# Optimization experiments

Measured on AMD Instinct MI355X. Metric: run time of the kernel, lower is better.

The kernel has to match this reference:

```python
import jax, jax.numpy as jnp
import numpy as np

N_NODES = 16384


def gcn_conv(x, W, b, src, dst, n):
    # PyG GCNConv: h = D^{-1/2} (A + I) D^{-1/2} (x W) + b, edge weights = 1
    h = x @ W  # [N, C_out]
    ones = jnp.ones(src.shape[0], dtype=x.dtype)
    deg = jax.ops.segment_sum(ones, dst, num_segments=n) + 1.0  # +1 for self-loop
    inv_sqrt = jax.lax.rsqrt(deg)
    coef = inv_sqrt[src] * inv_sqrt[dst]  # [E]
    agg = jax.ops.segment_sum(h[src] * coef[:, None], dst, num_segments=n)
    agg = agg + h * (inv_sqrt * inv_sqrt)[:, None]  # self-loop term
    return agg + b


def setup_inputs() -> dict:
    key = jax.random.key(0)
    k_x, k_e, k_w1, k_w2 = jax.random.split(key, 4)
    n, e = N_NODES, 524288
    c_in, c_hid, c_out = 128, 64, 16
    x = jax.random.normal(k_x, (n, c_in), dtype=jnp.float32)
    edge_index = jax.random.randint(k_e, (2, e), 0, n, dtype=jnp.int64)
    adj = jnp.zeros((n, n), dtype=jnp.float32)  # unused in forward (only in loss())
    s1 = 1.0 / np.sqrt(c_in)
    s2 = 1.0 / np.sqrt(c_hid)
    W1 = jax.random.uniform(k_w1, (c_in, c_hid), minval=-s1, maxval=s1, dtype=jnp.float32)
    b1 = jnp.zeros((c_hid,), dtype=jnp.float32)
    W2 = jax.random.uniform(k_w2, (c_hid, c_out), minval=-s2, maxval=s2, dtype=jnp.float32)
    b2 = jnp.zeros((c_out,), dtype=jnp.float32)
    return {"x": x, "edge_index": edge_index, "adj": adj,
            "W1": W1, "b1": b1, "W2": W2, "b2": b2}


def reference(x, edge_index, adj, W1, b1, W2, b2):
    n = x.shape[0]
    src, dst = edge_index[0], edge_index[1]
    h = jax.nn.relu(gcn_conv(x, W1, b1, src, dst, n))
    logits = gcn_conv(h, W2, b2, src, dst, n)
    return jax.nn.softmax(logits, axis=1)
```

## Files before the change

### kernel.cpp

```cpp
#include <hip/hip_runtime.h>
#include <math.h>

#define N_NODES 16384
#define N_EDGES 524288
#define C_IN    128
#define C_HID   64
#define C_OUT   16
#define CAP     128

__global__ __launch_bounds__(256) void k_gemm1_bin(const float* __restrict__ x,
                                                   const float* __restrict__ W1,
                                                   float* __restrict__ h1,
                                                   const int* __restrict__ src,
                                                   const int* __restrict__ dst,
                                                   int* __restrict__ cnt,
                                                   int* __restrict__ csr) {
    __shared__ float sW[C_IN][C_HID];
    __shared__ float sx[16][C_IN];
    int tid = threadIdx.x;
    int e = (blockIdx.x * 256 + tid) * 2;

    int2 s2 = *(const int2*)&src[e];
    int2 d2 = *(const int2*)&dst[e];
    int slot0 = atomicAdd(&cnt[d2.x], 1);
    int slot1 = atomicAdd(&cnt[d2.y], 1);
    if (slot0 < CAP) csr[d2.x * CAP + slot0] = s2.x;
    if (slot1 < CAP) csr[d2.y * CAP + slot1] = s2.y;

    const float4* W4 = (const float4*)W1;
    float4* sW4 = (float4*)sW;
    for (int i = tid; i < C_IN * C_HID / 4; i += 256) sW4[i] = W4[i];
    const float4* x4 = (const float4*)(x + (size_t)blockIdx.x * 16 * C_IN);
    float4* sx4 = (float4*)sx;
    for (int i = tid; i < 16 * C_IN / 4; i += 256) sx4[i] = x4[i];
    __syncthreads();

    int w = tid >> 6, col = tid & 63;
    float a0 = 0.f, a1 = 0.f, a2 = 0.f, a3 = 0.f;
#pragma unroll 8
    for (int k = 0; k < C_IN; ++k) {
        float wv = sW[k][col];
        a0 = fmaf(sx[w][k],      wv, a0);
        a1 = fmaf(sx[w + 4][k],  wv, a1);
        a2 = fmaf(sx[w + 8][k],  wv, a2);
        a3 = fmaf(sx[w + 12][k], wv, a3);
    }
    int node0 = blockIdx.x * 16;
    h1[(node0 + w) * C_HID + col]      = a0;
    h1[(node0 + w + 4) * C_HID + col]  = a1;
    h1[(node0 + w + 8) * C_HID + col]  = a2;
    h1[(node0 + w + 12) * C_HID + col] = a3;
}

__global__ __launch_bounds__(256) void k_l1(const float* __restrict__ h1,
                                            const int* __restrict__ csr,
                                            const int* __restrict__ cnt,
                                            const float* __restrict__ b1,
                                            const float* __restrict__ W2,
                                            float* __restrict__ h2) {
    __shared__ float sW[C_OUT][C_HID + 1];
    __shared__ float sz[4][C_HID];
    int tid = threadIdx.x;
    for (int i = tid; i < C_HID * C_OUT; i += 256) {
        int k = i >> 4, c = i & 15;
        sW[c][k] = W2[i];
    }
    __syncthreads();

    int w = tid >> 6, lane = tid & 63;
    int node = blockIdx.x * 4 + w;
    int degf = cnt[node];
    int deg = degf < CAP ? degf : CAP;
    int sub = lane >> 4;
    int cq  = lane & 15;
    int cbase = node * CAP;

    float4 acc = make_float4(0.f, 0.f, 0.f, 0.f);
    for (int j = sub; j < deg; j += 4) {
        int s = csr[cbase + j];
        float iv = rsqrtf((float)cnt[s] + 1.0f);
        const float4 v = *(const float4*)&h1[s * C_HID + 4 * cq];
        acc.x = fmaf(v.x, iv, acc.x);
        acc.y = fmaf(v.y, iv, acc.y);
        acc.z = fmaf(v.z, iv, acc.z);
        acc.w = fmaf(v.w, iv, acc.w);
    }
    acc.x += __shfl_xor(acc.x, 16); acc.y += __shfl_xor(acc.y, 16);
    acc.z += __shfl_xor(acc.z, 16); acc.w += __shfl_xor(acc.w, 16);
    acc.x += __shfl_xor(acc.x, 32); acc.y += __shfl_xor(acc.y, 32);
    acc.z += __shfl_xor(acc.z, 32); acc.w += __shfl_xor(acc.w, 32);

    float ivd = rsqrtf((float)degf + 1.0f);
    float iv2 = ivd * ivd;
    const float4 self = *(const float4*)&h1[node * C_HID + 4 * cq];
    const float4 bb   = *(const float4*)&b1[4 * cq];
    if (lane < 16) {
        sz[w][4 * cq]     = fmaxf(fmaf(acc.x, ivd, fmaf(self.x, iv2, bb.x)), 0.f);
        sz[w][4 * cq + 1] = fmaxf(fmaf(acc.y, ivd, fmaf(self.y, iv2, bb.y)), 0.f);
        sz[w][4 * cq + 2] = fmaxf(fmaf(acc.z, ivd, fmaf(self.z, iv2, bb.z)), 0.f);
        sz[w][4 * cq + 3] = fmaxf(fmaf(acc.w, ivd, fmaf(self.w, iv2, bb.w)), 0.f);
    }
    int c = lane & 15, kg = lane >> 4;
    float p = 0.f;
#pragma unroll
    for (int i = 0; i < 16; ++i) {
        int k = kg * 16 + i;
        p += sz[w][k] * sW[c][k];
    }
    p += __shfl_xor(p, 16);
    p += __shfl_xor(p, 32);
    if (kg == 0) h2[node * C_OUT + c] = p;
}

__global__ __launch_bounds__(256) void k_l2(const float* __restrict__ h2,
                                            const int* __restrict__ csr,
                                            const int* __restrict__ cnt,
                                            const float* __restrict__ b2,
                                            float* __restrict__ out) {
    int tid = threadIdx.x;
    int w = tid >> 6, lane = tid & 63;
    int node = blockIdx.x * 4 + w;
    int degf = cnt[node];
    int deg = degf < CAP ? degf : CAP;
    int g  = lane >> 2;
    int cq = lane & 3;
    int cbase = node * CAP;

    float4 acc = make_float4(0.f, 0.f, 0.f, 0.f);
    for (int j = g; j < deg; j += 16) {
        int s = csr[cbase + j];
        float iv = rsqrtf((float)cnt[s] + 1.0f);
        const float4 v = *(const float4*)&h2[s * C_OUT + 4 * cq];
        acc.x = fmaf(v.x, iv, acc.x);
        acc.y = fmaf(v.y, iv, acc.y);
        acc.z = fmaf(v.z, iv, acc.z);
        acc.w = fmaf(v.w, iv, acc.w);
    }
#pragma unroll
    for (int d = 4; d < 64; d <<= 1) {
        acc.x += __shfl_xor(acc.x, d); acc.y += __shfl_xor(acc.y, d);
        acc.z += __shfl_xor(acc.z, d); acc.w += __shfl_xor(acc.w, d);
    }

    float ivd = rsqrtf((float)degf + 1.0f);
    float iv2 = ivd * ivd;
    const float4 self = *(const float4*)&h2[node * C_OUT + 4 * cq];
    const float4 bb   = *(const float4*)&b2[4 * cq];
    float l0  = fmaf(acc.x, ivd, fmaf(self.x, iv2, bb.x));
    float l1v = fmaf(acc.y, ivd, fmaf(self.y, iv2, bb.y));
    float l2v = fmaf(acc.z, ivd, fmaf(self.z, iv2, bb.z));
    float l3  = fmaf(acc.w, ivd, fmaf(self.w, iv2, bb.w));

    float mx = fmaxf(fmaxf(l0, l1v), fmaxf(l2v, l3));
    mx = fmaxf(mx, __shfl_xor(mx, 1));
    mx = fmaxf(mx, __shfl_xor(mx, 2));
    float e0 = expf(l0 - mx), e1 = expf(l1v - mx);
    float e2 = expf(l2v - mx), e3 = expf(l3 - mx);
    float sum = e0 + e1 + e2 + e3;
    sum += __shfl_xor(sum, 1);
    sum += __shfl_xor(sum, 2);
    float r = 1.0f / sum;
    if (lane < 4) {
        float4 o = make_float4(e0 * r, e1 * r, e2 * r, e3 * r);
        *(float4*)&out[node * C_OUT + 4 * cq] = o;
    }
}

extern "C" void kernel_launch(void* const* d_in, const int* in_sizes, int n_in,
                              void* d_out, int out_size, void* d_ws, size_t ws_size,
                              hipStream_t stream) {
    const float* x    = (const float*)d_in[0];
    const int*   eidx = (const int*)d_in[1];
    const float* W1   = (const float*)d_in[3];
    const float* b1   = (const float*)d_in[4];
    const float* W2   = (const float*)d_in[5];
    const float* b2   = (const float*)d_in[6];
    float* out = (float*)d_out;

    const int* src = eidx;
    const int* dst = eidx + N_EDGES;

    char* ws = (char*)d_ws;
    int*   cnt = (int*)  (ws);
    int*   csr = (int*)  (ws + (1 << 20));
    float* h1  = (float*)(ws + (16 << 20));
    float* h2  = (float*)(ws + (24 << 20));

    hipMemsetAsync(cnt, 0, (size_t)N_NODES * sizeof(int), stream);

    k_gemm1_bin<<<N_NODES / 16, 256, 0, stream>>>(x, W1, h1, src, dst, cnt, csr);
    k_l1<<<N_NODES / 4, 256, 0, stream>>>(h1, csr, cnt, b1, W2, h2);
    k_l2<<<N_NODES / 4, 256, 0, stream>>>(h2, csr, cnt, b2, out);
}
```

Baseline: 73.74 us.

## Coarsen GEMM/binning and aggregation kernels, replace memset with zero kernel

The fused GEMM+edge-binning kernel now handles 4 edges per thread and 32 nodes per block, reusing each W1 element across 8 rows. The two aggregation kernels loop over 4 groups of nodes per block, so there are fewer blocks and the W2 shared-memory staging is amortised. The memset is replaced by a small zeroing kernel. The aim is to cut per-block setup, W1 reloads and launch overhead, at the cost of fewer blocks, so less parallelism for hiding gather latency.

```diff
diff --git a/kernel.cpp b/kernel.cpp
--- a/kernel.cpp
+++ b/kernel.cpp
@@ -7,6 +7,10 @@
 #define C_HID   64
 #define C_OUT   16
 #define CAP     128
+
+__global__ __launch_bounds__(256) void k_zero(int4* __restrict__ cnt4) {
+    cnt4[blockIdx.x * 256 + threadIdx.x] = make_int4(0, 0, 0, 0);
+}
 
 __global__ __launch_bounds__(256) void k_gemm1_bin(const float* __restrict__ x,
                                                    const float* __restrict__ W1,
@@ -16,40 +20,42 @@
                                                    int* __restrict__ cnt,
                                                    int* __restrict__ csr) {
     __shared__ float sW[C_IN][C_HID];
-    __shared__ float sx[16][C_IN];
+    __shared__ float sx[32][C_IN];
     int tid = threadIdx.x;
-    int e = (blockIdx.x * 256 + tid) * 2;
-
-    int2 s2 = *(const int2*)&src[e];
-    int2 d2 = *(const int2*)&dst[e];
-    int slot0 = atomicAdd(&cnt[d2.x], 1);
-    int slot1 = atomicAdd(&cnt[d2.y], 1);
-    if (slot0 < CAP) csr[d2.x * CAP + slot0] = s2.x;
-    if (slot1 < CAP) csr[d2.y * CAP + slot1] = s2.y;
+    int e = (blockIdx.x * 256 + tid) * 4;
+
+    int4 s4 = *(const int4*)&src[e];
+    int4 d4 = *(const int4*)&dst[e];
+    int sl0 = atomicAdd(&cnt[d4.x], 1);
+    int sl1 = atomicAdd(&cnt[d4.y], 1);
+    int sl2 = atomicAdd(&cnt[d4.z], 1);
+    int sl3 = atomicAdd(&cnt[d4.w], 1);
+    if (sl0 < CAP) csr[d4.x * CAP + sl0] = s4.x;
+    if (sl1 < CAP) csr[d4.y * CAP + sl1] = s4.y;
+    if (sl2 < CAP) csr[d4.z * CAP + sl2] = s4.z;
+    if (sl3 < CAP) csr[d4.w * CAP + sl3] = s4.w;
 
     const float4* W4 = (const float4*)W1;
     float4* sW4 = (float4*)sW;
     for (int i = tid; i < C_IN * C_HID / 4; i += 256) sW4[i] = W4[i];
-    const float4* x4 = (const float4*)(x + (size_t)blockIdx.x * 16 * C_IN);
+    const float4* x4 = (const float4*)(x + (size_t)blockIdx.x * 32 * C_IN);
     float4* sx4 = (float4*)sx;
-    for (int i = tid; i < 16 * C_IN / 4; i += 256) sx4[i] = x4[i];
+    for (int i = tid; i < 32 * C_IN / 4; i += 256) sx4[i] = x4[i];
     __syncthreads();
 
     int w = tid >> 6, col = tid & 63;
-    float a0 = 0.f, a1 = 0.f, a2 = 0.f, a3 = 0.f;
-#pragma unroll 8
+    float a[8] = {0.f, 0.f, 0.f, 0.f, 0.f, 0.f, 0.f, 0.f};
+#pragma unroll 4
     for (int k = 0; k < C_IN; ++k) {
         float wv = sW[k][col];
-        a0 = fmaf(sx[w][k],      wv, a0);
-        a1 = fmaf(sx[w + 4][k],  wv, a1);
-        a2 = fmaf(sx[w + 8][k],  wv, a2);
-        a3 = fmaf(sx[w + 12][k], wv, a3);
-    }
-    int node0 = blockIdx.x * 16;
-    h1[(node0 + w) * C_HID + col]      = a0;
-    h1[(node0 + w + 4) * C_HID + col]  = a1;
-    h1[(node0 + w + 8) * C_HID + col]  = a2;
-    h1[(node0 + w + 12) * C_HID + col] = a3;
+#pragma unroll
+        for (int i = 0; i < 8; ++i)
+            a[i] = fmaf(sx[w + 4 * i][k], wv, a[i]);
+    }
+    int node0 = blockIdx.x * 32;
+#pragma unroll
+    for (int i = 0; i < 8; ++i)
+        h1[(node0 + w + 4 * i) * C_HID + col] = a[i];
 }
 
 __global__ __launch_bounds__(256) void k_l1(const float* __restrict__ h1,
@@ -68,48 +74,51 @@
     __syncthreads();
 
     int w = tid >> 6, lane = tid & 63;
-    int node = blockIdx.x * 4 + w;
-    int degf = cnt[node];
-    int deg = degf < CAP ? degf : CAP;
     int sub = lane >> 4;
     int cq  = lane & 15;
-    int cbase = node * CAP;
-
-    float4 acc = make_float4(0.f, 0.f, 0.f, 0.f);
-    for (int j = sub; j < deg; j += 4) {
-        int s = csr[cbase + j];
-        float iv = rsqrtf((float)cnt[s] + 1.0f);
-        const float4 v = *(const float4*)&h1[s * C_HID + 4 * cq];
-        acc.x = fmaf(v.x, iv, acc.x);
-        acc.y = fmaf(v.y, iv, acc.y);
-        acc.z = fmaf(v.z, iv, acc.z);
-        acc.w = fmaf(v.w, iv, acc.w);
-    }
-    acc.x += __shfl_xor(acc.x, 16); acc.y += __shfl_xor(acc.y, 16);
-    acc.z += __shfl_xor(acc.z, 16); acc.w += __shfl_xor(acc.w, 16);
-    acc.x += __shfl_xor(acc.x, 32); acc.y += __shfl_xor(acc.y, 32);
-    acc.z += __shfl_xor(acc.z, 32); acc.w += __shfl_xor(acc.w, 32);
-
-    float ivd = rsqrtf((float)degf + 1.0f);
-    float iv2 = ivd * ivd;
-    const float4 self = *(const float4*)&h1[node * C_HID + 4 * cq];
-    const float4 bb   = *(const float4*)&b1[4 * cq];
-    if (lane < 16) {
-        sz[w][4 * cq]     = fmaxf(fmaf(acc.x, ivd, fmaf(self.x, iv2, bb.x)), 0.f);
-        sz[w][4 * cq + 1] = fmaxf(fmaf(acc.y, ivd, fmaf(self.y, iv2, bb.y)), 0.f);
-        sz[w][4 * cq + 2] = fmaxf(fmaf(acc.z, ivd, fmaf(self.z, iv2, bb.z)), 0.f);
-        sz[w][4 * cq + 3] = fmaxf(fmaf(acc.w, ivd, fmaf(self.w, iv2, bb.w)), 0.f);
-    }
     int c = lane & 15, kg = lane >> 4;
-    float p = 0.f;
-#pragma unroll
-    for (int i = 0; i < 16; ++i) {
-        int k = kg * 16 + i;
-        p += sz[w][k] * sW[c][k];
-    }
-    p += __shfl_xor(p, 16);
-    p += __shfl_xor(p, 32);
-    if (kg == 0) h2[node * C_OUT + c] = p;
+
+    for (int it = 0; it < 4; ++it) {
+        int node = blockIdx.x * 16 + it * 4 + w;
+        int degf = cnt[node];
+        int deg = degf < CAP ? degf : CAP;
+        int cbase = node * CAP;
+
+        float4 acc = make_float4(0.f, 0.f, 0.f, 0.f);
+        for (int j = sub; j < deg; j += 4) {
+            int s = csr[cbase + j];
+            float iv = rsqrtf((float)cnt[s] + 1.0f);
+            const float4 v = *(const float4*)&h1[s * C_HID + 4 * cq];
+            acc.x = fmaf(v.x, iv, acc.x);
+            acc.y = fmaf(v.y, iv, acc.y);
+            acc.z = fmaf(v.z, iv, acc.z);
+            acc.w = fmaf(v.w, iv, acc.w);
+        }
+        acc.x += __shfl_xor(acc.x, 16); acc.y += __shfl_xor(acc.y, 16);
+        acc.z += __shfl_xor(acc.z, 16); acc.w += __shfl_xor(acc.w, 16);
+        acc.x += __shfl_xor(acc.x, 32); acc.y += __shfl_xor(acc.y, 32);
+        acc.z += __shfl_xor(acc.z, 32); acc.w += __shfl_xor(acc.w, 32);
+
+        float ivd = rsqrtf((float)degf + 1.0f);
+        float iv2 = ivd * ivd;
+        const float4 self = *(const float4*)&h1[node * C_HID + 4 * cq];
+        const float4 bb   = *(const float4*)&b1[4 * cq];
+        if (lane < 16) {
+            sz[w][4 * cq]     = fmaxf(fmaf(acc.x, ivd, fmaf(self.x, iv2, bb.x)), 0.f);
+            sz[w][4 * cq + 1] = fmaxf(fmaf(acc.y, ivd, fmaf(self.y, iv2, bb.y)), 0.f);
+            sz[w][4 * cq + 2] = fmaxf(fmaf(acc.z, ivd, fmaf(self.z, iv2, bb.z)), 0.f);
+            sz[w][4 * cq + 3] = fmaxf(fmaf(acc.w, ivd, fmaf(self.w, iv2, bb.w)), 0.f);
+        }
+        float p = 0.f;
+#pragma unroll
+        for (int i = 0; i < 16; ++i) {
+            int k = kg * 16 + i;
+            p += sz[w][k] * sW[c][k];
+        }
+        p += __shfl_xor(p, 16);
+        p += __shfl_xor(p, 32);
+        if (kg == 0) h2[node * C_OUT + c] = p;
+    }
 }
 
 __global__ __launch_bounds__(256) void k_l2(const float* __restrict__ h2,
@@ -119,50 +128,53 @@
                                             float* __restrict__ out) {
     int tid = threadIdx.x;
     int w = tid >> 6, lane = tid & 63;
-    int node = blockIdx.x * 4 + w;
-    int degf = cnt[node];
-    int deg = degf < CAP ? degf : CAP;
     int g  = lane >> 2;
     int cq = lane & 3;
-    int cbase = node * CAP;
-
-    float4 acc = make_float4(0.f, 0.f, 0.f, 0.f);
-    for (int j = g; j < deg; j += 16) {
-        int s = csr[cbase + j];
-        float iv = rsqrtf((float)cnt[s] + 1.0f);
-        const float4 v = *(const float4*)&h2[s * C_OUT + 4 * cq];
-        acc.x = fmaf(v.x, iv, acc.x);
-        acc.y = fmaf(v.y, iv, acc.y);
-        acc.z = fmaf(v.z, iv, acc.z);
-        acc.w = fmaf(v.w, iv, acc.w);
-    }
-#pragma unroll
-    for (int d = 4; d < 64; d <<= 1) {
-        acc.x += __shfl_xor(acc.x, d); acc.y += __shfl_xor(acc.y, d);
-        acc.z += __shfl_xor(acc.z, d); acc.w += __shfl_xor(acc.w, d);
-    }
-
-    float ivd = rsqrtf((float)degf + 1.0f);
-    float iv2 = ivd * ivd;
-    const float4 self = *(const float4*)&h2[node * C_OUT + 4 * cq];
-    const float4 bb   = *(const float4*)&b2[4 * cq];
-    float l0  = fmaf(acc.x, ivd, fmaf(self.x, iv2, bb.x));
-    float l1v = fmaf(acc.y, ivd, fmaf(self.y, iv2, bb.y));
-    float l2v = fmaf(acc.z, ivd, fmaf(self.z, iv2, bb.z));
-    float l3  = fmaf(acc.w, ivd, fmaf(self.w, iv2, bb.w));
-
-    float mx = fmaxf(fmaxf(l0, l1v), fmaxf(l2v, l3));
-    mx = fmaxf(mx, __shfl_xor(mx, 1));
-    mx = fmaxf(mx, __shfl_xor(mx, 2));
-    float e0 = expf(l0 - mx), e1 = expf(l1v - mx);
-    float e2 = expf(l2v - mx), e3 = expf(l3 - mx);
-    float sum = e0 + e1 + e2 + e3;
-    sum += __shfl_xor(sum, 1);
-    sum += __shfl_xor(sum, 2);
-    float r = 1.0f / sum;
-    if (lane < 4) {
-        float4 o = make_float4(e0 * r, e1 * r, e2 * r, e3 * r);
-        *(float4*)&out[node * C_OUT + 4 * cq] = o;
+
+    for (int it = 0; it < 4; ++it) {
+        int node = blockIdx.x * 16 + it * 4 + w;
+        int degf = cnt[node];
+        int deg = degf < CAP ? degf : CAP;
+        int cbase = node * CAP;
+
+        float4 acc = make_float4(0.f, 0.f, 0.f, 0.f);
+        for (int j = g; j < deg; j += 16) {
+            int s = csr[cbase + j];
+            float iv = rsqrtf((float)cnt[s] + 1.0f);
+            const float4 v = *(const float4*)&h2[s * C_OUT + 4 * cq];
+            acc.x = fmaf(v.x, iv, acc.x);
+            acc.y = fmaf(v.y, iv, acc.y);
+            acc.z = fmaf(v.z, iv, acc.z);
+            acc.w = fmaf(v.w, iv, acc.w);
+        }
+#pragma unroll
+        for (int d = 4; d < 64; d <<= 1) {
+            acc.x += __shfl_xor(acc.x, d); acc.y += __shfl_xor(acc.y, d);
+            acc.z += __shfl_xor(acc.z, d); acc.w += __shfl_xor(acc.w, d);
+        }
+
+        float ivd = rsqrtf((float)degf + 1.0f);
+        float iv2 = ivd * ivd;
+        const float4 self = *(const float4*)&h2[node * C_OUT + 4 * cq];
+        const float4 bb   = *(const float4*)&b2[4 * cq];
+        float l0  = fmaf(acc.x, ivd, fmaf(self.x, iv2, bb.x));
+        float l1v = fmaf(acc.y, ivd, fmaf(self.y, iv2, bb.y));
+        float l2v = fmaf(acc.z, ivd, fmaf(self.z, iv2, bb.z));
+        float l3  = fmaf(acc.w, ivd, fmaf(self.w, iv2, bb.w));
+
+        float mx = fmaxf(fmaxf(l0, l1v), fmaxf(l2v, l3));
+        mx = fmaxf(mx, __shfl_xor(mx, 1));
+        mx = fmaxf(mx, __shfl_xor(mx, 2));
+        float e0 = expf(l0 - mx), e1 = expf(l1v - mx);
+        float e2 = expf(l2v - mx), e3 = expf(l3 - mx);
+        float sum = e0 + e1 + e2 + e3;
+        sum += __shfl_xor(sum, 1);
+        sum += __shfl_xor(sum, 2);
+        float r = 1.0f / sum;
+        if (lane < 4) {
+            float4 o = make_float4(e0 * r, e1 * r, e2 * r, e3 * r);
+            *(float4*)&out[node * C_OUT + 4 * cq] = o;
+        }
     }
 }
 
@@ -186,9 +198,8 @@
     float* h1  = (float*)(ws + (16 << 20));
     float* h2  = (float*)(ws + (24 << 20));
 
-    hipMemsetAsync(cnt, 0, (size_t)N_NODES * sizeof(int), stream);
-
-    k_gemm1_bin<<<N_NODES / 16, 256, 0, stream>>>(x, W1, h1, src, dst, cnt, csr);
-    k_l1<<<N_NODES / 4, 256, 0, stream>>>(h1, csr, cnt, b1, W2, h2);
-    k_l2<<<N_NODES / 4, 256, 0, stream>>>(h2, csr, cnt, b2, out);
-}
+    k_zero<<<16, 256, 0, stream>>>((int4*)cnt);
+    k_gemm1_bin<<<N_NODES / 32, 256, 0, stream>>>(x, W1, h1, src, dst, cnt, csr);
+    k_l1<<<N_NODES / 16, 256, 0, stream>>>(h1, csr, cnt, b1, W2, h2);
+    k_l2<<<N_NODES / 16, 256, 0, stream>>>(h2, csr, cnt, b2, out);
+}
```

Measured after the change: 83.66 us. 1.13x slower.
